# Kernel optimization log

Hardware: AMD Instinct MI355X
Metric: run time of the kernel (lower is better)

Reference implementation:

```python
import jax, jax.numpy as jnp
import numpy as np
import math

PHI = (1.0 + math.sqrt(5.0)) / 2.0
LUT_SIZE = 4096
D_MODEL = 2048
BATCH = 8192
TWO_PI = 2.0 * math.pi


def lut_sin_cos(theta, sin_table, cos_table):
    """LUT-based sin/cos with linear interpolation over [0, 2*pi)."""
    n = sin_table.shape[0]
    pos = jnp.mod(theta, TWO_PI) * (n / TWO_PI)        # [B, D] in [0, n)
    i0f = jnp.floor(pos)
    frac = pos - i0f
    i0 = i0f.astype(jnp.int32) % n
    i1 = (i0 + 1) % n
    s = sin_table[i0] * (1.0 - frac) + sin_table[i1] * frac
    c = cos_table[i0] * (1.0 - frac) + cos_table[i1] * frac
    return s, c


def setup_inputs() -> dict:
    key = jax.random.key(0)
    ks = jax.random.split(key, 6)
    x_real = jax.random.normal(ks[0], (BATCH, D_MODEL), dtype=jnp.float32)
    x_imag = jax.random.normal(ks[1], (BATCH, D_MODEL), dtype=jnp.float32)
    t = jax.random.uniform(ks[2], (BATCH,), dtype=jnp.float32)
    memory_real = jnp.zeros((BATCH, D_MODEL), dtype=jnp.float32)
    memory_imag = jnp.zeros((BATCH, D_MODEL), dtype=jnp.float32)
    w_trigger = jax.random.normal(ks[3], (D_MODEL,), dtype=jnp.float32) * 0.02
    b_trigger = jnp.zeros((D_MODEL,), dtype=jnp.float32)
    w_state = jax.random.normal(ks[4], (D_MODEL,), dtype=jnp.float32) * 0.02
    b_state = jnp.zeros((D_MODEL,), dtype=jnp.float32)
    k = jnp.asarray(3.0, dtype=jnp.float32)
    grid = jnp.arange(LUT_SIZE, dtype=jnp.float32) * (TWO_PI / LUT_SIZE)
    sin_table = jnp.sin(grid)
    cos_table = jnp.cos(grid)
    return dict(x_real=x_real, x_imag=x_imag, t=t,
                memory_real=memory_real, memory_imag=memory_imag,
                w_trigger=w_trigger, b_trigger=b_trigger,
                w_state=w_state, b_state=b_state, k=k,
                sin_table=sin_table, cos_table=cos_table)


def reference(x_real, x_imag, t, memory_real, memory_imag,
              w_trigger, b_trigger, w_state, b_state, k,
              sin_table, cos_table):
    scale = math.sqrt(x_real.shape[-1])
    t_phi = t[:, None] * PHI                                  # [B, 1]

    # trigger phase
    wl_trigger = 1.0 + jnp.abs(w_trigger)
    theta_tr = x_real / wl_trigger + b_trigger + t_phi
    theta_ti = x_imag / wl_trigger + b_trigger + t_phi
    sin_tr, cos_tr = lut_sin_cos(theta_tr, sin_table, cos_table)
    sin_ti, cos_ti = lut_sin_cos(theta_ti, sin_table, cos_table)
    trigger_real = cos_tr * cos_ti - sin_tr * sin_ti
    trigger_imag = cos_tr * sin_ti + sin_tr * cos_ti

    # interference -> exponential decay gate
    interference_raw = jnp.sum(trigger_real * x_real + trigger_imag * x_imag, axis=-1)
    interference_clamped = jnp.clip(interference_raw / scale, -1.0, 1.0)
    x_inv = (1.0 - interference_clamped) / 2.0
    k_eff = jnp.abs(k) + 0.1
    alpha = jnp.exp(-k_eff * x_inv)[:, None]                  # [B, 1]

    # blend with (detached) memory, then re-evolve
    blended_real = alpha * x_real + (1.0 - alpha) * memory_real
    blended_imag = alpha * x_imag + (1.0 - alpha) * memory_imag
    wl_state = 1.0 + jnp.abs(w_state)
    theta_sr = blended_real / wl_state + b_state + t_phi
    theta_si = blended_imag / wl_state + b_state + t_phi
    sin_sr, cos_sr = lut_sin_cos(theta_sr, sin_table, cos_table)
    sin_si, cos_si = lut_sin_cos(theta_si, sin_table, cos_table)
    evolved_real = cos_sr * cos_si - sin_sr * sin_si
    evolved_imag = cos_sr * sin_si + sin_sr * cos_si
    return evolved_real, evolved_imag
```

## Files before the change

kernel.cpp:

```cpp
#include <hip/hip_runtime.h>

#define DMODEL   2048
#define NTHREADS 256

typedef float fx4 __attribute__((ext_vector_type(4)));

__device__ __forceinline__ void fast_sincos(float theta, float& s, float& c) {
    const float INV_TWO_PI = 0.15915494309189535f;
    float r  = theta * INV_TWO_PI;
    float rr = r - floorf(r);
#if __has_builtin(__builtin_amdgcn_sinf) && __has_builtin(__builtin_amdgcn_cosf)
    s = __builtin_amdgcn_sinf(rr);
    c = __builtin_amdgcn_cosf(rr);
#else
    s = __sinf(rr * 6.283185307179586f);
    c = __cosf(rr * 6.283185307179586f);
#endif
}

__device__ __forceinline__ float fast_rcp(float x) {
#if __has_builtin(__builtin_amdgcn_rcpf)
    return __builtin_amdgcn_rcpf(x);
#else
    return 1.0f / x;
#endif
}

template <typename T>
__device__ __forceinline__ void nt_store(T v, T* p) {
#if __has_builtin(__builtin_nontemporal_store)
    __builtin_nontemporal_store(v, p);
#else
    *p = v;
#endif
}

__global__ __launch_bounds__(NTHREADS)
void liquid_echo_kernel(const float* __restrict__ x_real,
                        const float* __restrict__ x_imag,
                        const float* __restrict__ tvec,
                        const float* __restrict__ memory_real,
                        const float* __restrict__ memory_imag,
                        const float* __restrict__ w_trigger,
                        const float* __restrict__ b_trigger,
                        const float* __restrict__ w_state,
                        const float* __restrict__ b_state,
                        const float* __restrict__ kptr,
                        float* __restrict__ out,
                        size_t imag_off)
{
    __shared__ float red[NTHREADS / 64];

    const int tid = threadIdx.x;
    const int row = blockIdx.x;

    const float t_phi = tvec[row] * 1.6180339887498948f;
    const int c0 = tid * 4;
    const int c1 = (DMODEL / 2) + tid * 4;
    const size_t rb = (size_t)row * DMODEL;

    fx4 xr0 = *(const fx4*)(x_real + rb + c0);
    fx4 xr1 = *(const fx4*)(x_real + rb + c1);
    fx4 xi0 = *(const fx4*)(x_imag + rb + c0);
    fx4 xi1 = *(const fx4*)(x_imag + rb + c1);
    fx4 mr0 = *(const fx4*)(memory_real + rb + c0);
    fx4 mr1 = *(const fx4*)(memory_real + rb + c1);
    fx4 mi0 = *(const fx4*)(memory_imag + rb + c0);
    fx4 mi1 = *(const fx4*)(memory_imag + rb + c1);

    float sxy[8];
    float smm[8];
    float partial = 0.0f;
    {
        const fx4 wt0 = *(const fx4*)(w_trigger + c0);
        const fx4 wt1 = *(const fx4*)(w_trigger + c1);
        const fx4 bt0 = *(const fx4*)(b_trigger + c0);
        const fx4 bt1 = *(const fx4*)(b_trigger + c1);
        #pragma unroll
        for (int j = 0; j < 4; ++j) {
            float iw   = fast_rcp(1.0f + fabsf(wt0[j]));
            float base = bt0[j] + t_phi;
            float sx   = xr0[j] + xi0[j];
            sxy[j]     = sx;
            smm[j]     = mr0[j] + mi0[j];
            float ths  = fmaf(sx, iw, base + base);
            float s, c;
            fast_sincos(ths, s, c);
            partial = fmaf(c, xr0[j], partial);
            partial = fmaf(s, xi0[j], partial);
        }
        #pragma unroll
        for (int j = 0; j < 4; ++j) {
            float iw   = fast_rcp(1.0f + fabsf(wt1[j]));
            float base = bt1[j] + t_phi;
            float sx   = xr1[j] + xi1[j];
            sxy[4 + j] = sx;
            smm[4 + j] = mr1[j] + mi1[j];
            float ths  = fmaf(sx, iw, base + base);
            float s, c;
            fast_sincos(ths, s, c);
            partial = fmaf(c, xr1[j], partial);
            partial = fmaf(s, xi1[j], partial);
        }
    }

    #pragma unroll
    for (int off = 32; off > 0; off >>= 1)
        partial += __shfl_down(partial, off, 64);
    if ((tid & 63) == 0) red[tid >> 6] = partial;
    __syncthreads();

    float tot   = red[0] + red[1] + red[2] + red[3];
    float ic    = tot * (1.0f / 45.254833995939045f);
    ic          = fminf(1.0f, fmaxf(-1.0f, ic));
    float x_inv = (1.0f - ic) * 0.5f;
    float k_eff = fabsf(kptr[0]) + 0.1f;
    const float alpha = __expf(-k_eff * x_inv);
    const float oma   = 1.0f - alpha;

    float* outr = out + rb;
    float* outi = out + imag_off + rb;

    {
        const fx4 ws0 = *(const fx4*)(w_state + c0);
        const fx4 ws1 = *(const fx4*)(w_state + c1);
        const fx4 bs0 = *(const fx4*)(b_state + c0);
        const fx4 bs1 = *(const fx4*)(b_state + c1);
        fx4 er, ei;
        #pragma unroll
        for (int j = 0; j < 4; ++j) {
            float sb   = fmaf(alpha, sxy[j], oma * smm[j]);
            float iw   = fast_rcp(1.0f + fabsf(ws0[j]));
            float base = bs0[j] + t_phi;
            float ths  = fmaf(sb, iw, base + base);
            float s, c;
            fast_sincos(ths, s, c);
            er[j] = c;
            ei[j] = s;
        }
        nt_store(er, (fx4*)(outr + c0));
        nt_store(ei, (fx4*)(outi + c0));
        #pragma unroll
        for (int j = 0; j < 4; ++j) {
            float sb   = fmaf(alpha, sxy[4 + j], oma * smm[4 + j]);
            float iw   = fast_rcp(1.0f + fabsf(ws1[j]));
            float base = bs1[j] + t_phi;
            float ths  = fmaf(sb, iw, base + base);
            float s, c;
            fast_sincos(ths, s, c);
            er[j] = c;
            ei[j] = s;
        }
        nt_store(er, (fx4*)(outr + c1));
        nt_store(ei, (fx4*)(outi + c1));
    }
}

extern "C" void kernel_launch(void* const* d_in, const int* in_sizes, int n_in,
                              void* d_out, int out_size, void* d_ws, size_t ws_size,
                              hipStream_t stream) {
    const float* x_real      = (const float*)d_in[0];
    const float* x_imag      = (const float*)d_in[1];
    const float* t           = (const float*)d_in[2];
    const float* memory_real = (const float*)d_in[3];
    const float* memory_imag = (const float*)d_in[4];
    const float* w_trigger   = (const float*)d_in[5];
    const float* b_trigger   = (const float*)d_in[6];
    const float* w_state     = (const float*)d_in[7];
    const float* b_state     = (const float*)d_in[8];
    const float* k           = (const float*)d_in[9];
    float* out = (float*)d_out;

    int B = in_sizes[0] / DMODEL;
    size_t imag_off = (size_t)out_size / 2;

    liquid_echo_kernel<<<B, NTHREADS, 0, stream>>>(
        x_real, x_imag, t, memory_real, memory_imag,
        w_trigger, b_trigger, w_state, b_state, k,
        out, imag_off);
}
```

Before: 335.2 us.

## Process four rows per block with software prefetch of next row

Each block now handles four consecutive rows instead of one. The loads for row i+1 are issued right after the trigger pass of row i, so they overlap that row's reduction and state-evolution work. The reduction buffer is double-buffered so only one raw s_barrier is needed per row, and k_eff is hoisted out of the loop. The grid shrinks fourfold (2048 blocks), which lowers occupancy-driven latency hiding and raises register pressure from the prefetched vectors.

```diff
diff --git a/kernel.cpp b/kernel.cpp
--- a/kernel.cpp
+++ b/kernel.cpp
@@ -2,6 +2,7 @@
 
 #define DMODEL   2048
 #define NTHREADS 256
+#define ROWS_PER_BLK 4
 
 typedef float fx4 __attribute__((ext_vector_type(4)));
 
@@ -47,112 +48,143 @@
                         const float* __restrict__ b_state,
                         const float* __restrict__ kptr,
                         float* __restrict__ out,
+                        int nrows,
                         size_t imag_off)
 {
-    __shared__ float red[NTHREADS / 64];
+    __shared__ float red[2][NTHREADS / 64];
 
     const int tid = threadIdx.x;
-    const int row = blockIdx.x;
-
-    const float t_phi = tvec[row] * 1.6180339887498948f;
-    const int c0 = tid * 4;
-    const int c1 = (DMODEL / 2) + tid * 4;
-    const size_t rb = (size_t)row * DMODEL;
-
-    fx4 xr0 = *(const fx4*)(x_real + rb + c0);
-    fx4 xr1 = *(const fx4*)(x_real + rb + c1);
-    fx4 xi0 = *(const fx4*)(x_imag + rb + c0);
-    fx4 xi1 = *(const fx4*)(x_imag + rb + c1);
-    fx4 mr0 = *(const fx4*)(memory_real + rb + c0);
-    fx4 mr1 = *(const fx4*)(memory_real + rb + c1);
-    fx4 mi0 = *(const fx4*)(memory_imag + rb + c0);
-    fx4 mi1 = *(const fx4*)(memory_imag + rb + c1);
-
-    float sxy[8];
-    float smm[8];
-    float partial = 0.0f;
+    const int c0  = tid * 4;
+    const int c1  = (DMODEL / 2) + tid * 4;
+    const int row0 = blockIdx.x * ROWS_PER_BLK;
+
+    const float k_eff = fabsf(kptr[0]) + 0.1f;
+
+    fx4 xr0, xr1, xi0, xi1, mr0, mr1, mi0, mi1;
+    float t_next;
+
     {
-        const fx4 wt0 = *(const fx4*)(w_trigger + c0);
-        const fx4 wt1 = *(const fx4*)(w_trigger + c1);
-        const fx4 bt0 = *(const fx4*)(b_trigger + c0);
-        const fx4 bt1 = *(const fx4*)(b_trigger + c1);
+        const size_t rb = (size_t)row0 * DMODEL;
+        xr0 = *(const fx4*)(x_real + rb + c0);
+        xr1 = *(const fx4*)(x_real + rb + c1);
+        xi0 = *(const fx4*)(x_imag + rb + c0);
+        xi1 = *(const fx4*)(x_imag + rb + c1);
+        mr0 = *(const fx4*)(memory_real + rb + c0);
+        mr1 = *(const fx4*)(memory_real + rb + c1);
+        mi0 = *(const fx4*)(memory_imag + rb + c0);
+        mi1 = *(const fx4*)(memory_imag + rb + c1);
+        t_next = tvec[row0];
+    }
+
+    #pragma unroll
+    for (int i = 0; i < ROWS_PER_BLK; ++i) {
+        const int row = row0 + i;
+        if (row >= nrows) break;
+
+        const size_t rb   = (size_t)row * DMODEL;
+        const float t_phi = t_next * 1.6180339887498948f;
+
+        float sxy[8], smm[8];
+        float partial = 0.0f;
+        {
+            const fx4 wt0 = *(const fx4*)(w_trigger + c0);
+            const fx4 wt1 = *(const fx4*)(w_trigger + c1);
+            const fx4 bt0 = *(const fx4*)(b_trigger + c0);
+            const fx4 bt1 = *(const fx4*)(b_trigger + c1);
+            #pragma unroll
+            for (int j = 0; j < 4; ++j) {
+                float iw   = fast_rcp(1.0f + fabsf(wt0[j]));
+                float base = bt0[j] + t_phi;
+                float sx   = xr0[j] + xi0[j];
+                sxy[j]     = sx;
+                smm[j]     = mr0[j] + mi0[j];
+                float ths  = fmaf(sx, iw, base + base);
+                float s, c;
+                fast_sincos(ths, s, c);
+                partial = fmaf(c, xr0[j], partial);
+                partial = fmaf(s, xi0[j], partial);
+            }
+            #pragma unroll
+            for (int j = 0; j < 4; ++j) {
+                float iw   = fast_rcp(1.0f + fabsf(wt1[j]));
+                float base = bt1[j] + t_phi;
+                float sx   = xr1[j] + xi1[j];
+                sxy[4 + j] = sx;
+                smm[4 + j] = mr1[j] + mi1[j];
+                float ths  = fmaf(sx, iw, base + base);
+                float s, c;
+                fast_sincos(ths, s, c);
+                partial = fmaf(c, xr1[j], partial);
+                partial = fmaf(s, xi1[j], partial);
+            }
+        }
+
+        if (i + 1 < ROWS_PER_BLK && row + 1 < nrows) {
+            const size_t rb2 = (size_t)(row + 1) * DMODEL;
+            xr0 = *(const fx4*)(x_real + rb2 + c0);
+            xr1 = *(const fx4*)(x_real + rb2 + c1);
+            xi0 = *(const fx4*)(x_imag + rb2 + c0);
+            xi1 = *(const fx4*)(x_imag + rb2 + c1);
+            mr0 = *(const fx4*)(memory_real + rb2 + c0);
+            mr1 = *(const fx4*)(memory_real + rb2 + c1);
+            mi0 = *(const fx4*)(memory_imag + rb2 + c0);
+            mi1 = *(const fx4*)(memory_imag + rb2 + c1);
+            t_next = tvec[row + 1];
+        }
+
         #pragma unroll
-        for (int j = 0; j < 4; ++j) {
-            float iw   = fast_rcp(1.0f + fabsf(wt0[j]));
-            float base = bt0[j] + t_phi;
-            float sx   = xr0[j] + xi0[j];
-            sxy[j]     = sx;
-            smm[j]     = mr0[j] + mi0[j];
-            float ths  = fmaf(sx, iw, base + base);
-            float s, c;
-            fast_sincos(ths, s, c);
-            partial = fmaf(c, xr0[j], partial);
-            partial = fmaf(s, xi0[j], partial);
+        for (int off = 32; off > 0; off >>= 1)
+            partial += __shfl_down(partial, off, 64);
+        if ((tid & 63) == 0) red[i & 1][tid >> 6] = partial;
+
+        asm volatile("s_waitcnt lgkmcnt(0)" ::: "memory");
+        __builtin_amdgcn_s_barrier();
+        asm volatile("" ::: "memory");
+
+        float tot = red[i & 1][0] + red[i & 1][1]
+                  + red[i & 1][2] + red[i & 1][3];
+        float ic    = tot * (1.0f / 45.254833995939045f);
+        ic          = fminf(1.0f, fmaxf(-1.0f, ic));
+        float x_inv = (1.0f - ic) * 0.5f;
+        const float alpha = __expf(-k_eff * x_inv);
+        const float oma   = 1.0f - alpha;
+
+        float* outr = out + rb;
+        float* outi = out + imag_off + rb;
+
+        {
+            const fx4 ws0 = *(const fx4*)(w_state + c0);
+            const fx4 ws1 = *(const fx4*)(w_state + c1);
+            const fx4 bs0 = *(const fx4*)(b_state + c0);
+            const fx4 bs1 = *(const fx4*)(b_state + c1);
+            fx4 er, ei;
+            #pragma unroll
+            for (int j = 0; j < 4; ++j) {
+                float sb   = fmaf(alpha, sxy[j], oma * smm[j]);
+                float iw   = fast_rcp(1.0f + fabsf(ws0[j]));
+                float base = bs0[j] + t_phi;
+                float ths  = fmaf(sb, iw, base + base);
+                float s, c;
+                fast_sincos(ths, s, c);
+                er[j] = c;
+                ei[j] = s;
+            }
+            nt_store(er, (fx4*)(outr + c0));
+            nt_store(ei, (fx4*)(outi + c0));
+            #pragma unroll
+            for (int j = 0; j < 4; ++j) {
+                float sb   = fmaf(alpha, sxy[4 + j], oma * smm[4 + j]);
+                float iw   = fast_rcp(1.0f + fabsf(ws1[j]));
+                float base = bs1[j] + t_phi;
+                float ths  = fmaf(sb, iw, base + base);
+                float s, c;
+                fast_sincos(ths, s, c);
+                er[j] = c;
+                ei[j] = s;
+            }
+            nt_store(er, (fx4*)(outr + c1));
+            nt_store(ei, (fx4*)(outi + c1));
         }
-        #pragma unroll
-        for (int j = 0; j < 4; ++j) {
-            float iw   = fast_rcp(1.0f + fabsf(wt1[j]));
-            float base = bt1[j] + t_phi;
-            float sx   = xr1[j] + xi1[j];
-            sxy[4 + j] = sx;
-            smm[4 + j] = mr1[j] + mi1[j];
-            float ths  = fmaf(sx, iw, base + base);
-            float s, c;
-            fast_sincos(ths, s, c);
-            partial = fmaf(c, xr1[j], partial);
-            partial = fmaf(s, xi1[j], partial);
-        }
-    }
-
-    #pragma unroll
-    for (int off = 32; off > 0; off >>= 1)
-        partial += __shfl_down(partial, off, 64);
-    if ((tid & 63) == 0) red[tid >> 6] = partial;
-    __syncthreads();
-
-    float tot   = red[0] + red[1] + red[2] + red[3];
-    float ic    = tot * (1.0f / 45.254833995939045f);
-    ic          = fminf(1.0f, fmaxf(-1.0f, ic));
-    float x_inv = (1.0f - ic) * 0.5f;
-    float k_eff = fabsf(kptr[0]) + 0.1f;
-    const float alpha = __expf(-k_eff * x_inv);
-    const float oma   = 1.0f - alpha;
-
-    float* outr = out + rb;
-    float* outi = out + imag_off + rb;
-
-    {
-        const fx4 ws0 = *(const fx4*)(w_state + c0);
-        const fx4 ws1 = *(const fx4*)(w_state + c1);
-        const fx4 bs0 = *(const fx4*)(b_state + c0);
-        const fx4 bs1 = *(const fx4*)(b_state + c1);
-        fx4 er, ei;
-        #pragma unroll
-        for (int j = 0; j < 4; ++j) {
-            float sb   = fmaf(alpha, sxy[j], oma * smm[j]);
-            float iw   = fast_rcp(1.0f + fabsf(ws0[j]));
-            float base = bs0[j] + t_phi;
-            float ths  = fmaf(sb, iw, base + base);
-            float s, c;
-            fast_sincos(ths, s, c);
-            er[j] = c;
-            ei[j] = s;
-        }
-        nt_store(er, (fx4*)(outr + c0));
-        nt_store(ei, (fx4*)(outi + c0));
-        #pragma unroll
-        for (int j = 0; j < 4; ++j) {
-            float sb   = fmaf(alpha, sxy[4 + j], oma * smm[4 + j]);
-            float iw   = fast_rcp(1.0f + fabsf(ws1[j]));
-            float base = bs1[j] + t_phi;
-            float ths  = fmaf(sb, iw, base + base);
-            float s, c;
-            fast_sincos(ths, s, c);
-            er[j] = c;
-            ei[j] = s;
-        }
-        nt_store(er, (fx4*)(outr + c1));
-        nt_store(ei, (fx4*)(outi + c1));
     }
 }
 
@@ -173,9 +205,10 @@
 
     int B = in_sizes[0] / DMODEL;
     size_t imag_off = (size_t)out_size / 2;
-
-    liquid_echo_kernel<<<B, NTHREADS, 0, stream>>>(
+    int grid = (B + ROWS_PER_BLK - 1) / ROWS_PER_BLK;
+
+    liquid_echo_kernel<<<grid, NTHREADS, 0, stream>>>(
         x_real, x_imag, t, memory_real, memory_imag,
         w_trigger, b_trigger, w_state, b_state, k,
-        out, imag_off);
-}
+        out, B, imag_off);
+}
```

New measurement: 344.0 us. 2.6% more time.
